# Kernel optimization log

Hardware: AMD Instinct MI355X
Metric: run time of the kernel (lower is better)

Reference implementation:

```python
import jax, jax.numpy as jnp
import numpy as np

D_MODEL = 1024
N_HEADS = 16
HEAD_DIM = D_MODEL // N_HEADS
BLOCK_SIZE = 2048
B, T = 4, 2048


def setup_inputs() -> dict:
    key = jax.random.key(0)
    ks = jax.random.split(key, 5)
    s = 0.02
    x = jax.random.normal(ks[0], (B, T, D_MODEL), dtype=jnp.float32)
    W_qkv = jax.random.normal(ks[1], (D_MODEL, 3 * D_MODEL), dtype=jnp.float32) * s
    b_qkv = jnp.zeros((3 * D_MODEL,), dtype=jnp.float32)
    W_proj = jax.random.normal(ks[2], (D_MODEL, D_MODEL), dtype=jnp.float32) * s
    b_proj = jnp.zeros((D_MODEL,), dtype=jnp.float32)
    return {"x": x, "W_qkv": W_qkv, "b_qkv": b_qkv, "W_proj": W_proj, "b_proj": b_proj}


def reference(x, W_qkv, b_qkv, W_proj, b_proj):
    Bsz, Tlen, C = x.shape
    qkv = x @ W_qkv + b_qkv                      # [B,T,3C]
    q, k, v = jnp.split(qkv, 3, axis=2)
    # [B,T,C] -> [B,H,T,hd]
    def heads(t):
        return t.reshape(Bsz, Tlen, N_HEADS, HEAD_DIM).transpose(0, 2, 1, 3)
    q, k, v = heads(q), heads(k), heads(v)
    scale = 1.0 / jnp.sqrt(jnp.asarray(HEAD_DIM, dtype=x.dtype))
    att = jnp.einsum('bhqd,bhkd->bhqk', q, k) * scale   # [B,H,T,T]
    causal = jnp.tril(jnp.ones((Tlen, Tlen), dtype=bool))
    att = jnp.where(causal, att, jnp.asarray(-jnp.inf, dtype=att.dtype))
    att = jax.nn.softmax(att, axis=-1)
    y = jnp.einsum('bhqk,bhkd->bhqd', att, v)            # [B,H,T,hd]
    y = y.transpose(0, 2, 1, 3).reshape(Bsz, Tlen, C)
    return y @ W_proj + b_proj
```

## Files before the change

### kernel.cpp

```cpp
#include <hip/hip_runtime.h>
#include <hip/hip_bf16.h>

#define D_MODEL 1024
#define N_HEADS 16
#define HEAD_DIM 64
#define SEQ_T 2048
#define BATCH 4

#define SL2E 0.18033688011f

typedef short s8v  __attribute__((ext_vector_type(8)));
typedef float f32x4 __attribute__((ext_vector_type(4)));
typedef unsigned long long ull;

static __device__ __forceinline__ unsigned short f2bf(float f) {
  union { float f; unsigned int u; } v; v.f = f;
  unsigned int u = v.u;
  return (unsigned short)((u + 0x7FFF + ((u >> 16) & 1)) >> 16);
}
static __device__ __forceinline__ unsigned int fbits(float f) {
  union { float f; unsigned int u; } v; v.f = f; return v.u;
}

static __device__ __forceinline__ void glds16(const void* g, void* l) {
  __builtin_amdgcn_global_load_lds(
      (const __attribute__((address_space(1))) void*)g,
      (__attribute__((address_space(3))) void*)l, 16, 0, 0);
}

template<int MODE>
__global__ __launch_bounds__(256) void gemm_bt_kernel(
    const unsigned short* __restrict__ A, const unsigned short* __restrict__ Bt,
    const float* __restrict__ bias, float* __restrict__ Cout,
    unsigned short* __restrict__ qkb, unsigned short* __restrict__ vT,
    int M, int N, int K)
{
  __shared__ unsigned short Al[128 * 64];
  __shared__ unsigned short Bl[128 * 64];

  const int tid  = threadIdx.x;
  const int lane = tid & 63;
  const int wave = tid >> 6;
  const int col  = lane & 15;
  const int quad = lane >> 4;
  const int wm   = (wave & 1) * 64;
  const int wn   = (wave >> 1) * 64;
  const int bm0  = blockIdx.y * 128;
  const int bn0  = blockIdx.x * 128;
  const int cx   = col & 7;

  f32x4 acc[4][4];
  #pragma unroll
  for (int t = 0; t < 4; ++t)
    #pragma unroll
    for (int u = 0; u < 4; ++u) acc[t][u] = (f32x4)0.f;

  for (int k0 = 0; k0 < K; k0 += 64) {
    __syncthreads();
    #pragma unroll
    for (int i = 0; i < 4; ++i) {
      int idx = i * 256 + tid;
      int row = idx >> 3;
      int gc  = (idx & 7) ^ (row & 7);
      glds16(A  + (size_t)(bm0 + row) * K + k0 + gc * 8, &Al[idx * 8]);
      glds16(Bt + (size_t)(bn0 + row) * K + k0 + gc * 8, &Bl[idx * 8]);
    }
    __syncthreads();

    #pragma unroll
    for (int s = 0; s < 2; ++s) {
      s8v af[4], bf[4];
      #pragma unroll
      for (int t = 0; t < 4; ++t) {
        int ar = wm + t * 16 + col;
        af[t] = *(const s8v*)&Al[ar * 64 + (((s * 4 + quad) ^ cx) * 8)];
        int br = wn + t * 16 + col;
        bf[t] = *(const s8v*)&Bl[br * 64 + (((s * 4 + quad) ^ cx) * 8)];
      }
      #pragma unroll
      for (int t = 0; t < 4; ++t)
        #pragma unroll
        for (int u = 0; u < 4; ++u)
          acc[t][u] = __builtin_amdgcn_mfma_f32_16x16x32_bf16(
              af[t], bf[u], acc[t][u], 0, 0, 0);
    }
  }

  float bv[4];
  #pragma unroll
  for (int u = 0; u < 4; ++u) bv[u] = bias[bn0 + wn + u * 16 + col];

  if (MODE == 1 && bn0 >= 2048) {
    #pragma unroll
    for (int t = 0; t < 4; ++t) {
      int m_base = bm0 + wm + t * 16 + quad * 4;
      #pragma unroll
      for (int u = 0; u < 4; ++u) {
        int hd = (bn0 + wn + u * 16 + col) - 2048;
        size_t bh = (size_t)(bm0 >> 11) * 16 + (hd >> 6);
        ull pk = (ull)f2bf(acc[t][u][0] + bv[u])
               | ((ull)f2bf(acc[t][u][1] + bv[u]) << 16)
               | ((ull)f2bf(acc[t][u][2] + bv[u]) << 32)
               | ((ull)f2bf(acc[t][u][3] + bv[u]) << 48);
        *(ull*)(vT + (bh * 64 + (hd & 63)) * 2048 + (m_base & 2047)) = pk;
      }
    }
  } else {
    const float sc = (MODE == 1 && (bn0 + wn) < 1024) ? SL2E : 1.0f;
    #pragma unroll
    for (int t = 0; t < 4; ++t) {
      #pragma unroll
      for (int r = 0; r < 4; ++r) {
        size_t m = bm0 + wm + t * 16 + quad * 4 + r;
        #pragma unroll
        for (int u = 0; u < 4; ++u) {
          int n = bn0 + wn + u * 16 + col;
          float v = acc[t][u][r] + bv[u];
          if (MODE == 0) Cout[m * N + n] = v;
          else           qkb[m * 2048 + n] = f2bf(v * sc);
        }
      }
    }
  }
}

static __device__ __forceinline__ void transpose_tile(
    const float* __restrict__ W, unsigned short* __restrict__ Wt,
    int K, int N, int n0, int k0)
{
  __shared__ float tile[32][33];
  const int tx = threadIdx.x & 31, ty = threadIdx.x >> 5;
  #pragma unroll
  for (int i = 0; i < 4; ++i)
    tile[ty + i * 8][tx] = W[(size_t)(k0 + ty + i * 8) * N + n0 + tx];
  __syncthreads();
  #pragma unroll
  for (int i = 0; i < 4; ++i)
    Wt[(size_t)(n0 + ty + i * 8) * K + k0 + tx] = f2bf(tile[tx][ty + i * 8]);
}

__global__ __launch_bounds__(256) void prep_kernel(
    const float* __restrict__ x, const float* __restrict__ W_qkv,
    const float* __restrict__ W_proj, ushort4* __restrict__ xb,
    unsigned short* __restrict__ wqt, unsigned short* __restrict__ wpt)
{
  const int bid = blockIdx.x;
  if (bid < 8192) {
    int i = bid * 256 + threadIdx.x;
    float4 v = ((const float4*)x)[i];
    ushort4 o;
    o.x = f2bf(v.x); o.y = f2bf(v.y); o.z = f2bf(v.z); o.w = f2bf(v.w);
    xb[i] = o;
  } else if (bid < 8192 + 3072) {
    int b2 = bid - 8192;
    transpose_tile(W_qkv, wqt, 1024, 3072, (b2 % 96) * 32, (b2 / 96) * 32);
  } else {
    int b3 = bid - 11264;
    transpose_tile(W_proj, wpt, 1024, 1024, (b3 % 32) * 32, (b3 / 32) * 32);
  }
}

#define LPAD 72

__global__ __launch_bounds__(256, 3) void attn_mfma_kernel(
    const unsigned short* __restrict__ qk, const unsigned short* __restrict__ vT,
    unsigned short* __restrict__ y)
{
  __shared__ unsigned short Ks[2][64 * 64];
  __shared__ unsigned short Vs[2][64 * 64];
  __shared__ unsigned short Ps[128][LPAD];

  const int tid  = threadIdx.x;
  const int wave = tid >> 6;
  const int lane = tid & 63;
  const int col  = lane & 15;
  const int quad = lane >> 4;
  const int cx   = col & 7;

  const int bh = blockIdx.x;
  const int b = bh >> 4, h = bh & 15;
  const int qblk = 15 - (int)blockIdx.y;
  const int q0 = qblk * 128;
  const int nk = 2 * qblk + 2;
  const int C2 = 2048;

  const unsigned short* qbase = qk + (size_t)b * SEQ_T * C2 + h * 64;
  const unsigned short* kbase = qbase + 1024;
  const unsigned short* vbase = vT + (size_t)bh * 64 * 2048;

  s8v qf[2][2];
  #pragma unroll
  for (int s = 0; s < 2; ++s)
    #pragma unroll
    for (int c = 0; c < 2; ++c)
      qf[s][c] = *(const s8v*)(qbase +
          (size_t)(q0 + s * 64 + wave * 16 + col) * C2 + c * 32 + quad * 8);

  f32x4 acc[2][4];
  #pragma unroll
  for (int s = 0; s < 2; ++s)
    #pragma unroll
    for (int t = 0; t < 4; ++t) acc[s][t] = (f32x4)0.f;
  float lsum[2] = {0.f, 0.f};

  auto stage = [&](int kt, int bi) {
    const int k0 = kt * 64;
    #pragma unroll
    for (int i = 0; i < 2; ++i) {
      int cid = (i * 4 + wave) * 64 + lane;
      int row = cid >> 3;
      int gc  = (cid & 7) ^ (row & 7);
      glds16(kbase + (size_t)(k0 + row) * C2 + gc * 8, &Ks[bi][cid * 8]);
      glds16(vbase + (size_t)row * 2048 + k0 + gc * 8, &Vs[bi][cid * 8]);
    }
  };

  auto tile_body = [&](int kt, int bi) {
    const int k0 = kt * 64;

    s8v kf[4][2];
    #pragma unroll
    for (int t = 0; t < 4; ++t)
      #pragma unroll
      for (int c = 0; c < 2; ++c)
        kf[t][c] = *(const s8v*)&Ks[bi][(t * 16 + col) * 64 + (((c * 4 + quad) ^ cx) * 8)];

    #pragma unroll
    for (int s = 0; s < 2; ++s) {
      const int qs = q0 + s * 64 + wave * 16;
      if (k0 > qs + 15) continue;

      f32x4 st[4];
      #pragma unroll
      for (int t = 0; t < 4; ++t) st[t] = (f32x4)0.f;
      #pragma unroll
      for (int t = 0; t < 4; ++t)
        #pragma unroll
        for (int c = 0; c < 2; ++c)
          st[t] = __builtin_amdgcn_mfma_f32_16x16x32_bf16(kf[t][c], qf[s][c], st[t], 0, 0, 0);

      const bool diag = (k0 + 63 > qs);
      const int qg = qs + col;
      #pragma unroll
      for (int t = 0; t < 4; ++t) {
        float e[4];
        #pragma unroll
        for (int r = 0; r < 4; ++r) {
          float v = exp2f(st[t][r]);
          if (diag && (k0 + t * 16 + quad * 4 + r > qg)) v = 0.f;
          lsum[s] += v;
          e[r] = v;
        }
        uint2 pk;
        pk.x = ((fbits(e[0]) + 0x8000u) >> 16) | ((fbits(e[1]) + 0x8000u) & 0xFFFF0000u);
        pk.y = ((fbits(e[2]) + 0x8000u) >> 16) | ((fbits(e[3]) + 0x8000u) & 0xFFFF0000u);
        *(uint2*)&Ps[s * 64 + wave * 16 + col][t * 16 + quad * 4] = pk;
      }
    }

    s8v vf[4][2];
    #pragma unroll
    for (int t = 0; t < 4; ++t)
      #pragma unroll
      for (int c = 0; c < 2; ++c)
        vf[t][c] = *(const s8v*)&Vs[bi][(t * 16 + col) * 64 + (((c * 4 + quad) ^ cx) * 8)];
    #pragma unroll
    for (int s = 0; s < 2; ++s) {
      const int qs = q0 + s * 64 + wave * 16;
      if (k0 > qs + 15) continue;
      s8v pf[2];
      #pragma unroll
      for (int c = 0; c < 2; ++c)
        pf[c] = *(const s8v*)&Ps[s * 64 + wave * 16 + col][c * 32 + quad * 8];
      #pragma unroll
      for (int t = 0; t < 4; ++t)
        #pragma unroll
        for (int c = 0; c < 2; ++c)
          acc[s][t] = __builtin_amdgcn_mfma_f32_16x16x32_bf16(pf[c], vf[t][c], acc[s][t], 0, 0, 0);
    }
  };

  stage(0, 0);
  for (int kt = 0; kt < nk; kt += 2) {
    __syncthreads();
    if (kt + 1 < nk) stage(kt + 1, 1);
    tile_body(kt, 0);
    if (kt + 1 < nk) {
      __syncthreads();
      if (kt + 2 < nk) stage(kt + 2, 0);
      tile_body(kt + 1, 1);
    }
  }

  #pragma unroll
  for (int s = 0; s < 2; ++s) {
    float v = lsum[s];
    v += __shfl_xor(v, 16);
    v += __shfl_xor(v, 32);
    #pragma unroll
    for (int r = 0; r < 4; ++r) {
      float inv = 1.0f / __shfl(v, quad * 4 + r);
      int q = q0 + s * 64 + wave * 16 + quad * 4 + r;
      unsigned short* yrow = y + (size_t)(b * SEQ_T + q) * D_MODEL + h * 64;
      #pragma unroll
      for (int t = 0; t < 4; ++t)
        yrow[t * 16 + col] = f2bf(acc[s][t][r] * inv);
    }
  }
}

extern "C" void kernel_launch(void* const* d_in, const int* in_sizes, int n_in,
                              void* d_out, int out_size, void* d_ws, size_t ws_size,
                              hipStream_t stream) {
  const float* x      = (const float*)d_in[0];
  const float* W_qkv  = (const float*)d_in[1];
  const float* b_qkv  = (const float*)d_in[2];
  const float* W_proj = (const float*)d_in[3];
  const float* b_proj = (const float*)d_in[4];
  float* out = (float*)d_out;

  const int M  = BATCH * SEQ_T;
  const int C  = D_MODEL;
  const int C3 = 3 * D_MODEL;

  unsigned short* xb  = (unsigned short*)d_ws;
  unsigned short* wqt = xb  + (size_t)M * C;
  unsigned short* wpt = wqt + (size_t)C3 * C;
  unsigned short* qkb = wpt + (size_t)C * C;
  unsigned short* vTb = qkb + (size_t)M * 2 * C;
  unsigned short* yb  = vTb + (size_t)64 * 64 * SEQ_T;

  dim3 blk(256);

  prep_kernel<<<dim3(8192 + 3072 + 1024), blk, 0, stream>>>(
      x, W_qkv, W_proj, (ushort4*)xb, wqt, wpt);

  gemm_bt_kernel<1><<<dim3(C3 / 128, M / 128), blk, 0, stream>>>(
      xb, wqt, b_qkv, nullptr, qkb, vTb, M, C3, C);

  attn_mfma_kernel<<<dim3(BATCH * N_HEADS, SEQ_T / 128), blk, 0, stream>>>(
      qkb, vTb, yb);

  gemm_bt_kernel<0><<<dim3(C / 128, M / 128), blk, 0, stream>>>(
      yb, wpt, b_proj, out, nullptr, nullptr, M, C, C);
}
```

Before: 247.1 us.

## Vectorize epilogue stores, compute softmax sums via MFMA, swizzle P tile

The GEMM epilogues swap MFMA operand order so each lane holds four consecutive columns, which allows float4 and packed-bf16 vector stores instead of scalar ones. The QKV GEMM is split into two launches (QK and V-transpose) so the branch becomes a template parameter. In attention, the softmax row sums move from scalar adds plus shuffles to an extra MFMA against a ones vector, the P tile switches from padded to XOR-swizzled LDS layout, and the output store is vectorized. Packed hardware bf16 conversion replaces manual bit rounding where the builtin exists, which may change rounding slightly and adds MFMA work for the sums.

```diff
diff --git a/kernel.cpp b/kernel.cpp
--- a/kernel.cpp
+++ b/kernel.cpp
@@ -13,14 +13,26 @@
 typedef float f32x4 __attribute__((ext_vector_type(4)));
 typedef unsigned long long ull;
 
-static __device__ __forceinline__ unsigned short f2bf(float f) {
-  union { float f; unsigned int u; } v; v.f = f;
-  unsigned int u = v.u;
-  return (unsigned short)((u + 0x7FFF + ((u >> 16) & 1)) >> 16);
-}
 static __device__ __forceinline__ unsigned int fbits(float f) {
   union { float f; unsigned int u; } v; v.f = f; return v.u;
 }
+static __device__ __forceinline__ unsigned short f2bf(float f) {
+  unsigned int u = fbits(f);
+  return (unsigned short)((u + 0x7FFF + ((u >> 16) & 1)) >> 16);
+}
+
+#if __has_builtin(__builtin_amdgcn_cvt_pk_bf16_f32)
+typedef __bf16 bf2 __attribute__((ext_vector_type(2)));
+static __device__ __forceinline__ unsigned int pk2bf(float a, float b) {
+  union { bf2 v; unsigned int u; } u;
+  u.v = __builtin_amdgcn_cvt_pk_bf16_f32(a, b);
+  return u.u;
+}
+#else
+static __device__ __forceinline__ unsigned int pk2bf(float a, float b) {
+  return ((fbits(a) + 0x8000u) >> 16) | ((fbits(b) + 0x8000u) & 0xFFFF0000u);
+}
+#endif
 
 static __device__ __forceinline__ void glds16(const void* g, void* l) {
   __builtin_amdgcn_global_load_lds(
@@ -28,12 +40,12 @@
       (__attribute__((address_space(3))) void*)l, 16, 0, 0);
 }
 
-template<int MODE>
+template<int OUT>
 __global__ __launch_bounds__(256) void gemm_bt_kernel(
     const unsigned short* __restrict__ A, const unsigned short* __restrict__ Bt,
     const float* __restrict__ bias, float* __restrict__ Cout,
     unsigned short* __restrict__ qkb, unsigned short* __restrict__ vT,
-    int M, int N, int K)
+    int M, int N, int K, int bn_base)
 {
   __shared__ unsigned short Al[128 * 64];
   __shared__ unsigned short Bl[128 * 64];
@@ -46,7 +58,7 @@
   const int wm   = (wave & 1) * 64;
   const int wn   = (wave >> 1) * 64;
   const int bm0  = blockIdx.y * 128;
-  const int bn0  = blockIdx.x * 128;
+  const int bn0  = bn_base + blockIdx.x * 128;
   const int cx   = col & 7;
 
   f32x4 acc[4][4];
@@ -72,52 +84,53 @@
       s8v af[4], bf[4];
       #pragma unroll
       for (int t = 0; t < 4; ++t) {
-        int ar = wm + t * 16 + col;
-        af[t] = *(const s8v*)&Al[ar * 64 + (((s * 4 + quad) ^ cx) * 8)];
-        int br = wn + t * 16 + col;
-        bf[t] = *(const s8v*)&Bl[br * 64 + (((s * 4 + quad) ^ cx) * 8)];
+        af[t] = *(const s8v*)&Al[(wm + t * 16 + col) * 64 + (((s * 4 + quad) ^ cx) * 8)];
+        bf[t] = *(const s8v*)&Bl[(wn + t * 16 + col) * 64 + (((s * 4 + quad) ^ cx) * 8)];
       }
       #pragma unroll
       for (int t = 0; t < 4; ++t)
         #pragma unroll
-        for (int u = 0; u < 4; ++u)
-          acc[t][u] = __builtin_amdgcn_mfma_f32_16x16x32_bf16(
-              af[t], bf[u], acc[t][u], 0, 0, 0);
-    }
-  }
-
-  float bv[4];
-  #pragma unroll
-  for (int u = 0; u < 4; ++u) bv[u] = bias[bn0 + wn + u * 16 + col];
-
-  if (MODE == 1 && bn0 >= 2048) {
-    #pragma unroll
-    for (int t = 0; t < 4; ++t) {
-      int m_base = bm0 + wm + t * 16 + quad * 4;
-      #pragma unroll
-      for (int u = 0; u < 4; ++u) {
-        int hd = (bn0 + wn + u * 16 + col) - 2048;
+        for (int u = 0; u < 4; ++u) {
+          if (OUT == 2)
+            acc[t][u] = __builtin_amdgcn_mfma_f32_16x16x32_bf16(af[t], bf[u], acc[t][u], 0, 0, 0);
+          else
+            acc[t][u] = __builtin_amdgcn_mfma_f32_16x16x32_bf16(bf[u], af[t], acc[t][u], 0, 0, 0);
+        }
+    }
+  }
+
+  if (OUT == 2) {
+    #pragma unroll
+    for (int u = 0; u < 4; ++u) {
+      float bv = bias[bn0 + wn + u * 16 + col];
+      int hd = (bn0 + wn + u * 16 + col) - 2048;
+      #pragma unroll
+      for (int t = 0; t < 4; ++t) {
+        int m_base = bm0 + wm + t * 16 + quad * 4;
         size_t bh = (size_t)(bm0 >> 11) * 16 + (hd >> 6);
-        ull pk = (ull)f2bf(acc[t][u][0] + bv[u])
-               | ((ull)f2bf(acc[t][u][1] + bv[u]) << 16)
-               | ((ull)f2bf(acc[t][u][2] + bv[u]) << 32)
-               | ((ull)f2bf(acc[t][u][3] + bv[u]) << 48);
-        *(ull*)(vT + (bh * 64 + (hd & 63)) * 2048 + (m_base & 2047)) = pk;
+        uint2 pk;
+        pk.x = pk2bf(acc[t][u][0] + bv, acc[t][u][1] + bv);
+        pk.y = pk2bf(acc[t][u][2] + bv, acc[t][u][3] + bv);
+        *(uint2*)(vT + (bh * 64 + (hd & 63)) * 2048 + (m_base & 2047)) = pk;
       }
     }
   } else {
-    const float sc = (MODE == 1 && (bn0 + wn) < 1024) ? SL2E : 1.0f;
-    #pragma unroll
-    for (int t = 0; t < 4; ++t) {
-      #pragma unroll
-      for (int r = 0; r < 4; ++r) {
-        size_t m = bm0 + wm + t * 16 + quad * 4 + r;
-        #pragma unroll
-        for (int u = 0; u < 4; ++u) {
-          int n = bn0 + wn + u * 16 + col;
-          float v = acc[t][u][r] + bv[u];
-          if (MODE == 0) Cout[m * N + n] = v;
-          else           qkb[m * 2048 + n] = f2bf(v * sc);
+    const float sc = (OUT == 1 && bn0 < 1024) ? SL2E : 1.0f;
+    #pragma unroll
+    for (int u = 0; u < 4; ++u) {
+      int n_base = bn0 + wn + u * 16 + quad * 4;
+      float4 b4 = *(const float4*)&bias[n_base];
+      #pragma unroll
+      for (int t = 0; t < 4; ++t) {
+        size_t m = bm0 + wm + t * 16 + col;
+        float v0 = (acc[t][u][0] + b4.x) * sc, v1 = (acc[t][u][1] + b4.y) * sc;
+        float v2 = (acc[t][u][2] + b4.z) * sc, v3 = (acc[t][u][3] + b4.w) * sc;
+        if (OUT == 0) {
+          float4 o = {v0, v1, v2, v3};
+          *(float4*)(Cout + m * N + n_base) = o;
+        } else {
+          uint2 pk = {pk2bf(v0, v1), pk2bf(v2, v3)};
+          *(uint2*)(qkb + m * 2048 + n_base) = pk;
         }
       }
     }
@@ -141,15 +154,14 @@
 
 __global__ __launch_bounds__(256) void prep_kernel(
     const float* __restrict__ x, const float* __restrict__ W_qkv,
-    const float* __restrict__ W_proj, ushort4* __restrict__ xb,
+    const float* __restrict__ W_proj, uint2* __restrict__ xb,
     unsigned short* __restrict__ wqt, unsigned short* __restrict__ wpt)
 {
   const int bid = blockIdx.x;
   if (bid < 8192) {
     int i = bid * 256 + threadIdx.x;
     float4 v = ((const float4*)x)[i];
-    ushort4 o;
-    o.x = f2bf(v.x); o.y = f2bf(v.y); o.z = f2bf(v.z); o.w = f2bf(v.w);
+    uint2 o = {pk2bf(v.x, v.y), pk2bf(v.z, v.w)};
     xb[i] = o;
   } else if (bid < 8192 + 3072) {
     int b2 = bid - 8192;
@@ -160,15 +172,13 @@
   }
 }
 
-#define LPAD 72
-
 __global__ __launch_bounds__(256, 3) void attn_mfma_kernel(
     const unsigned short* __restrict__ qk, const unsigned short* __restrict__ vT,
     unsigned short* __restrict__ y)
 {
   __shared__ unsigned short Ks[2][64 * 64];
   __shared__ unsigned short Vs[2][64 * 64];
-  __shared__ unsigned short Ps[128][LPAD];
+  __shared__ unsigned short Ps[128 * 64];
 
   const int tid  = threadIdx.x;
   const int wave = tid >> 6;
@@ -188,6 +198,10 @@
   const unsigned short* kbase = qbase + 1024;
   const unsigned short* vbase = vT + (size_t)bh * 64 * 2048;
 
+  s8v ones;
+  #pragma unroll
+  for (int j = 0; j < 8; ++j) ones[j] = (short)0x3F80;
+
   s8v qf[2][2];
   #pragma unroll
   for (int s = 0; s < 2; ++s)
@@ -197,11 +211,13 @@
           (size_t)(q0 + s * 64 + wave * 16 + col) * C2 + c * 32 + quad * 8);
 
   f32x4 acc[2][4];
-  #pragma unroll
-  for (int s = 0; s < 2; ++s)
+  f32x4 accL[2];
+  #pragma unroll
+  for (int s = 0; s < 2; ++s) {
+    accL[s] = (f32x4)0.f;
     #pragma unroll
     for (int t = 0; t < 4; ++t) acc[s][t] = (f32x4)0.f;
-  float lsum[2] = {0.f, 0.f};
+  }
 
   auto stage = [&](int kt, int bi) {
     const int k0 = kt * 64;
@@ -217,6 +233,7 @@
 
   auto tile_body = [&](int kt, int bi) {
     const int k0 = kt * 64;
+    const int psrow = wave * 16 + col;
 
     s8v kf[4][2];
     #pragma unroll
@@ -248,13 +265,11 @@
         for (int r = 0; r < 4; ++r) {
           float v = exp2f(st[t][r]);
           if (diag && (k0 + t * 16 + quad * 4 + r > qg)) v = 0.f;
-          lsum[s] += v;
           e[r] = v;
         }
-        uint2 pk;
-        pk.x = ((fbits(e[0]) + 0x8000u) >> 16) | ((fbits(e[1]) + 0x8000u) & 0xFFFF0000u);
-        pk.y = ((fbits(e[2]) + 0x8000u) >> 16) | ((fbits(e[3]) + 0x8000u) & 0xFFFF0000u);
-        *(uint2*)&Ps[s * 64 + wave * 16 + col][t * 16 + quad * 4] = pk;
+        uint2 pk = {pk2bf(e[0], e[1]), pk2bf(e[2], e[3])};
+        *(uint2*)&Ps[(s * 64 + psrow) * 64 +
+                     (((2 * t + (quad >> 1)) ^ cx) * 8) + (quad & 1) * 4] = pk;
       }
     }
 
@@ -271,12 +286,15 @@
       s8v pf[2];
       #pragma unroll
       for (int c = 0; c < 2; ++c)
-        pf[c] = *(const s8v*)&Ps[s * 64 + wave * 16 + col][c * 32 + quad * 8];
+        pf[c] = *(const s8v*)&Ps[(s * 64 + psrow) * 64 + (((c * 4 + quad) ^ cx) * 8)];
+      #pragma unroll
+      for (int c = 0; c < 2; ++c)
+        accL[s] = __builtin_amdgcn_mfma_f32_16x16x32_bf16(ones, pf[c], accL[s], 0, 0, 0);
       #pragma unroll
       for (int t = 0; t < 4; ++t)
         #pragma unroll
         for (int c = 0; c < 2; ++c)
-          acc[s][t] = __builtin_amdgcn_mfma_f32_16x16x32_bf16(pf[c], vf[t][c], acc[s][t], 0, 0, 0);
+          acc[s][t] = __builtin_amdgcn_mfma_f32_16x16x32_bf16(vf[t][c], pf[c], acc[s][t], 0, 0, 0);
     }
   };
 
@@ -294,17 +312,14 @@
 
   #pragma unroll
   for (int s = 0; s < 2; ++s) {
-    float v = lsum[s];
-    v += __shfl_xor(v, 16);
-    v += __shfl_xor(v, 32);
-    #pragma unroll
-    for (int r = 0; r < 4; ++r) {
-      float inv = 1.0f / __shfl(v, quad * 4 + r);
-      int q = q0 + s * 64 + wave * 16 + quad * 4 + r;
-      unsigned short* yrow = y + (size_t)(b * SEQ_T + q) * D_MODEL + h * 64;
-      #pragma unroll
-      for (int t = 0; t < 4; ++t)
-        yrow[t * 16 + col] = f2bf(acc[s][t][r] * inv);
+    float inv = 1.0f / accL[s][0];
+    int q = q0 + s * 64 + wave * 16 + col;
+    unsigned short* yrow = y + (size_t)(b * SEQ_T + q) * D_MODEL + h * 64 + quad * 4;
+    #pragma unroll
+    for (int t = 0; t < 4; ++t) {
+      uint2 pk = {pk2bf(acc[s][t][0] * inv, acc[s][t][1] * inv),
+                  pk2bf(acc[s][t][2] * inv, acc[s][t][3] * inv)};
+      *(uint2*)(yrow + t * 16) = pk;
     }
   }
 }
@@ -333,14 +348,16 @@
   dim3 blk(256);
 
   prep_kernel<<<dim3(8192 + 3072 + 1024), blk, 0, stream>>>(
-      x, W_qkv, W_proj, (ushort4*)xb, wqt, wpt);
-
-  gemm_bt_kernel<1><<<dim3(C3 / 128, M / 128), blk, 0, stream>>>(
-      xb, wqt, b_qkv, nullptr, qkb, vTb, M, C3, C);
+      x, W_qkv, W_proj, (uint2*)xb, wqt, wpt);
+
+  gemm_bt_kernel<1><<<dim3(16, M / 128), blk, 0, stream>>>(
+      xb, wqt, b_qkv, nullptr, qkb, nullptr, M, 2048, C, 0);
+  gemm_bt_kernel<2><<<dim3(8, M / 128), blk, 0, stream>>>(
+      xb, wqt, b_qkv, nullptr, nullptr, vTb, M, C3, C, 2048);
 
   attn_mfma_kernel<<<dim3(BATCH * N_HEADS, SEQ_T / 128), blk, 0, stream>>>(
       qkb, vTb, yb);
 
-  gemm_bt_kernel<0><<<dim3(C / 128, M / 128), blk, 0, stream>>>(
-      yb, wpt, b_proj, out, nullptr, nullptr, M, C, C);
-}
+  gemm_bt_kernel<0><<<dim3(8, M / 128), blk, 0, stream>>>(
+      yb, wpt, b_proj, out, nullptr, nullptr, M, C, C, 0);
+}
```

Result: slower. 267.7 us (+8.3%).
